# Optimization experiments

Hardware: AMD Instinct MI355X
Metric: run time of the kernel (lower is better)

Reference implementation:

```python
import jax, jax.numpy as jnp
import numpy as np

NUM_BANDS = 8
WINDOW = 2048
OVERLAP = 1024
SR = 16000


def _band_mask(L):
    # Replicates torch: band = searchsorted(band_ranges, |freq|, left) - 1.
    # DC bin gives band=-1 which torch negative-indexes into the LAST band,
    # hence the mod. All bins satisfy band < NUM_BANDS, so all are assigned.
    freqs = np.fft.fftfreq(L, 1.0 / SR)
    ranges = np.linspace(0.0, SR / 2.0, NUM_BANDS + 1)
    idx = np.searchsorted(ranges, np.abs(freqs), side='left') - 1
    idx = idx % NUM_BANDS
    mask = (idx[None, :] == np.arange(NUM_BANDS)[:, None]).astype(np.float32)
    return jnp.asarray(mask)  # [bands, L]


def _band_signals(x):
    # mag*exp(i*phase) of masked bins == masked complex bins; ifft().real per band
    L = x.shape[-1]
    X = jnp.fft.fft(x)                         # [B, L] complex
    mask = _band_mask(L)                       # [bands, L]
    Xb = X[:, None, :] * mask[None, :, :]      # [B, bands, L]
    return jnp.fft.ifft(Xb).real               # [B, bands, L]


def _chunks(sig):
    L = sig.shape[-1]
    hop = WINDOW - OVERLAP
    n = (L - OVERLAP) // hop                   # num_chunks (static)
    idx = (jnp.arange(n) * hop)[:, None] + jnp.arange(WINDOW)[None, :]  # [n, W]
    return sig[:, :, idx]                       # [B, bands, n, W]


def _loudness(x):
    # BS.1770-style energy loudness (vectorized stand-in for the repo's
    # undefined `loudness` helper): -0.691 + 10*log10(mean square)
    ms = jnp.mean(x * x, axis=-1)
    return -0.691 + 10.0 * jnp.log10(ms + 1e-12)


def reference(watermarked_signals, original_signals):
    ro = _band_signals(original_signals)
    rw = _band_signals(watermarked_signals)
    lo = _loudness(_chunks(ro))                # [B, bands, n]
    lw = _loudness(_chunks(rw))
    lo = jnp.where(jnp.isnan(lo), 0.0, lo)
    lw = jnp.where(jnp.isnan(lw), 0.0, lw)
    diff = (lw - lo).reshape(-1)               # ordered (i, j, k) like the torch loop
    w = jax.nn.softmax(diff)
    return jnp.sum(w * diff)


def setup_inputs() -> dict:
    key = jax.random.key(0)
    k1, k2 = jax.random.split(key)
    B, L = 8, 160000
    return {
        'watermarked_signals': jax.random.normal(k1, (B, L), dtype=jnp.float32),
        'original_signals': jax.random.normal(k2, (B, L), dtype=jnp.float32),
    }
```

## Files before the change

kernel.cpp:

```cpp
#include <hip/hip_runtime.h>
#include <hip/hip_fp16.h>
#include <math.h>

constexpr int L      = 160000;
constexpr int BATCH  = 8;
constexpr int NB     = 8;
constexpr int NHOPS  = 156;
constexpr int NCHUNK = 155;
constexpr int RS     = 289;
constexpr float TWO_PI = 6.28318530717958647692f;
constexpr float INVL = 1.0f / (float)L;

__device__ __forceinline__ float2 cmulf(float2 a, float2 b) {
  return make_float2(a.x * b.x - a.y * b.y, a.x * b.y + a.y * b.x);
}

__device__ __forceinline__ float2 cisf(float a) {
  float s, c;
  __sincosf(a, &s, &c);
  return make_float2(c, s);
}

__device__ __forceinline__ int pad8(int i) { return i + (i >> 3); }

template <int SIGN>
__device__ __forceinline__ void bf4s(float2* v) {
  float2 t0 = make_float2(v[0].x + v[2].x, v[0].y + v[2].y);
  float2 t1 = make_float2(v[0].x - v[2].x, v[0].y - v[2].y);
  float2 t2 = make_float2(v[1].x + v[3].x, v[1].y + v[3].y);
  float2 t3 = make_float2(v[1].x - v[3].x, v[1].y - v[3].y);
  v[0] = make_float2(t0.x + t2.x, t0.y + t2.y);
  v[2] = make_float2(t0.x - t2.x, t0.y - t2.y);
  if constexpr (SIGN < 0) {
    v[1] = make_float2(t1.x + t3.y, t1.y - t3.x);
    v[3] = make_float2(t1.x - t3.y, t1.y + t3.x);
  } else {
    v[1] = make_float2(t1.x - t3.y, t1.y + t3.x);
    v[3] = make_float2(t1.x + t3.y, t1.y - t3.x);
  }
}

template <int SIGN>
__device__ __forceinline__ void bf5s(float2* v) {
  const float c1 = 0.30901699437494745f, s1 = 0.9510565162951535f;
  const float c2 = -0.8090169943749475f, s2 = 0.5877852522924731f;
  float2 t1 = make_float2(v[1].x + v[4].x, v[1].y + v[4].y);
  float2 t3 = make_float2(v[1].x - v[4].x, v[1].y - v[4].y);
  float2 t2 = make_float2(v[2].x + v[3].x, v[2].y + v[3].y);
  float2 t4 = make_float2(v[2].x - v[3].x, v[2].y - v[3].y);
  float2 a = make_float2(v[0].x + c1 * t1.x + c2 * t2.x, v[0].y + c1 * t1.y + c2 * t2.y);
  float2 b = make_float2(s1 * t3.x + s2 * t4.x, s1 * t3.y + s2 * t4.y);
  float2 c = make_float2(v[0].x + c2 * t1.x + c1 * t2.x, v[0].y + c2 * t1.y + c1 * t2.y);
  float2 d = make_float2(s2 * t3.x - s1 * t4.x, s2 * t3.y - s1 * t4.y);
  v[0] = make_float2(v[0].x + t1.x + t2.x, v[0].y + t1.y + t2.y);
  if constexpr (SIGN < 0) {
    v[1] = make_float2(a.x + b.y, a.y - b.x);
    v[4] = make_float2(a.x - b.y, a.y + b.x);
    v[2] = make_float2(c.x + d.y, c.y - d.x);
    v[3] = make_float2(c.x - d.y, c.y + d.x);
  } else {
    v[1] = make_float2(a.x - b.y, a.y + b.x);
    v[4] = make_float2(a.x + b.y, a.y - b.x);
    v[2] = make_float2(c.x - d.y, c.y + d.x);
    v[3] = make_float2(c.x + d.y, c.y - d.x);
  }
}

template <int R>
__device__ __forceinline__ void twchain(float2* v, float2 t1) {
  float2 t = t1;
  v[1] = cmulf(v[1], t);
#pragma unroll
  for (int r = 2; r < R; ++r) { t = cmulf(t, t1); v[r] = cmulf(v[r], t); }
}

__device__ __forceinline__ int rev3_5(int q) {
  int q5 = q / 5, q25 = q / 25;
  int d0 = q - 5 * q5, d1 = q5 - 5 * q25;
  return 25 * d0 + 5 * d1 + q25;
}

__device__ __forceinline__ int rev3_4(int q) {
  return ((q & 3) << 4) | (q & 12) | (q >> 4);
}

template <int SUB, int SIGN>
__device__ __forceinline__ void dif5_ip_stage_c(float2* a, int ln) {
  int i1 = ln, i2 = ln + 64;
  bool g2 = (i2 < 125);
  int j1 = i1 % SUB, j2 = i2 % SUB;
  int b1 = (i1 / SUB) * (5 * SUB) + j1;
  int b2 = (i2 / SUB) * (5 * SUB) + j2;
  float2 u[5], v[5];
#pragma unroll
  for (int r = 0; r < 5; ++r) u[r] = a[b1 + SUB * r];
  if (g2) {
#pragma unroll
    for (int r = 0; r < 5; ++r) v[r] = a[b2 + SUB * r];
  }
  bf5s<SIGN>(u);
  twchain<5>(u, cisf((float)SIGN * (TWO_PI / (float)(5 * SUB)) * (float)j1));
  if (g2) {
    bf5s<SIGN>(v);
    twchain<5>(v, cisf((float)SIGN * (TWO_PI / (float)(5 * SUB)) * (float)j2));
  }
#pragma unroll
  for (int r = 0; r < 5; ++r) a[b1 + SUB * r] = u[r];
  if (g2) {
#pragma unroll
    for (int r = 0; r < 5; ++r) a[b2 + SUB * r] = v[r];
  }
}

template <int SUB>
__device__ __forceinline__ void dif5_ip_stage_t(float2* a, int ln, float2 t1a, float2 t1b) {
  int i1 = ln, i2 = ln + 64;
  bool g2 = (i2 < 125);
  int j1 = i1 % SUB, j2 = i2 % SUB;
  int b1 = (i1 / SUB) * (5 * SUB) + j1;
  int b2 = (i2 / SUB) * (5 * SUB) + j2;
  float2 u[5], v[5];
#pragma unroll
  for (int r = 0; r < 5; ++r) u[r] = a[b1 + SUB * r];
  if (g2) {
#pragma unroll
    for (int r = 0; r < 5; ++r) v[r] = a[b2 + SUB * r];
  }
  bf5s<1>(u);
  twchain<5>(u, t1a);
  if (g2) {
    bf5s<1>(v);
    twchain<5>(v, t1b);
  }
#pragma unroll
  for (int r = 0; r < 5; ++r) a[b1 + SUB * r] = u[r];
  if (g2) {
#pragma unroll
    for (int r = 0; r < 5; ++r) a[b2 + SUB * r] = v[r];
  }
}

template <int SIGN>
__device__ __forceinline__ void dif625_ip(float2* a, int ln) {
  dif5_ip_stage_c<125, SIGN>(a, ln);
  dif5_ip_stage_c<25, SIGN>(a, ln);
  dif5_ip_stage_c<5, SIGN>(a, ln);
  int q1 = ln, q2 = ln + 64;
  bool g2 = (q2 < 125);
  float2 u[5], v[5];
#pragma unroll
  for (int r = 0; r < 5; ++r) u[r] = a[5 * q1 + r];
  if (g2) {
#pragma unroll
    for (int r = 0; r < 5; ++r) v[r] = a[5 * q2 + r];
  }
  bf5s<SIGN>(u);
  if (g2) bf5s<SIGN>(v);
  int rv1 = rev3_5(q1), rv2 = rev3_5(q2);
#pragma unroll
  for (int r = 0; r < 5; ++r) a[125 * r + rv1] = u[r];
  if (g2) {
#pragma unroll
    for (int r = 0; r < 5; ++r) a[125 * r + rv2] = v[r];
  }
}

template <int SIGN>
__device__ __forceinline__ void dif256sw_ip(float2* a, int ln) {
  {
    float2 u[4];
#pragma unroll
    for (int r = 0; r < 4; ++r) u[r] = a[pad8(ln + 64 * r)];
    bf4s<SIGN>(u);
    twchain<4>(u, cisf((float)SIGN * (TWO_PI / 256.0f) * (float)ln));
#pragma unroll
    for (int r = 0; r < 4; ++r) a[pad8(ln + 64 * r)] = u[r];
  }
  {
    int j = ln & 15, b = 64 * (ln >> 4) + j;
    float2 u[4];
#pragma unroll
    for (int r = 0; r < 4; ++r) u[r] = a[pad8(b + 16 * r)];
    bf4s<SIGN>(u);
    twchain<4>(u, cisf((float)SIGN * (TWO_PI / 64.0f) * (float)j));
#pragma unroll
    for (int r = 0; r < 4; ++r) a[pad8(b + 16 * r)] = u[r];
  }
  {
    int j = ln & 3, b = 16 * (ln >> 2) + j;
    float2 u[4];
#pragma unroll
    for (int r = 0; r < 4; ++r) u[r] = a[pad8(b + 4 * r)];
    bf4s<SIGN>(u);
    twchain<4>(u, cisf((float)SIGN * (TWO_PI / 16.0f) * (float)j));
#pragma unroll
    for (int r = 0; r < 4; ++r) a[pad8(b + 4 * r)] = u[r];
  }
  {
    float2 u[4];
#pragma unroll
    for (int r = 0; r < 4; ++r) u[r] = a[pad8(4 * ln + r)];
    bf4s<SIGN>(u);
    int rv = rev3_4(ln);
#pragma unroll
    for (int r = 0; r < 4; ++r) a[pad8(64 * r + rv)] = u[r];
  }
}

__global__ __launch_bounds__(256) void f1_kernel(const float* __restrict__ win,
                                                 const float* __restrict__ oin,
                                                 float2* __restrict__ G,
                                                 float* __restrict__ E) {
  __shared__ float2 A[4 * 625];
  int blk = blockIdx.x;
  int gid = blk * 256 + threadIdx.x;
  if (gid < 2 * BATCH * NB * NHOPS) E[gid] = 0.0f;
  int sig = blk >> 6, g = blk & 63;
  int n1base = g * 4;
  int tid = threadIdx.x;
  const float4* wp4 = (const float4*)(win + (size_t)sig * L);
  const float4* op4 = (const float4*)(oin + (size_t)sig * L);
  for (int r = tid; r < 625; r += 256) {
    float4 wv = wp4[r * 64 + g];
    float4 ov = op4[r * 64 + g];
    A[0 * 625 + r] = make_float2(wv.x, ov.x);
    A[1 * 625 + r] = make_float2(wv.y, ov.y);
    A[2 * 625 + r] = make_float2(wv.z, ov.z);
    A[3 * 625 + r] = make_float2(wv.w, ov.w);
  }
  __syncthreads();
  int wv_ = tid >> 6, ln = tid & 63;
  dif625_ip<-1>(A + wv_ * 625, ln);
  __syncthreads();
  int cc = tid & 3, k20 = tid >> 2;
  int n1 = n1base + cc;
  float w = -(TWO_PI / (float)L) * (float)n1;
  float2 t = cisf(w * (float)k20);
  float2 stp = cisf(w * 64.0f);
  for (int k2 = k20; k2 < 625; k2 += 64) {
    G[(size_t)sig * L + k2 * 256 + n1] = cmulf(A[cc * 625 + k2], t);
    t = cmulf(t, stp);
  }
}

__global__ __launch_bounds__(256) void f2_kernel(const float2* __restrict__ G,
                                                 float2* __restrict__ X) {
  __shared__ float2 A[4 * RS];
  int blk = blockIdx.x;
  int sig = blk / 157, gr = blk % 157;
  int k2base = gr * 4;
  int tid = threadIdx.x;
  int wv = tid >> 6, ln = tid & 63;
  int k2 = k2base + wv;
  float2* a = A + wv * RS;
  if (k2 < 625) {
#pragma unroll
    for (int r = 0; r < 4; ++r)
      a[pad8(ln + 64 * r)] = G[(size_t)sig * L + k2 * 256 + ln + 64 * r];
    dif256sw_ip<-1>(a, ln);
  }
  __syncthreads();
  for (int idx = tid; idx < 1024; idx += 256) {
    int row = idx >> 8, k1 = idx & 255;
    int k2e = k2base + row;
    if (k2e < 625) X[(size_t)sig * L + k2e * 256 + k1] = A[row * RS + pad8(k1)];
  }
}

__global__ __launch_bounds__(1024) void i1_kernel(const float2* __restrict__ X,
                                                  __half2* __restrict__ H) {
  __shared__ float2 A[16 * RS];
  int blk = blockIdx.x;
  int gr = blk % 40, sb = blk / 40;
  int band = sb & 7, sig = sb >> 3;
  int k2base = gr * 16;
  int tid = threadIdx.x;
  int wv = tid >> 6, ln = tid & 63;
  int lo1, hi1, lo2, hi2;
  if (band < 7) {
    lo1 = 10000 * band + 1;        hi1 = 10000 * (band + 1);
    lo2 = L - 10000 * (band + 1);  hi2 = L - 10000 * band - 1;
  } else {
    lo1 = 70001; hi1 = 80000; lo2 = 80001; hi2 = 89999;
  }
  float2 zero = make_float2(0.0f, 0.0f);
  int k2 = k2base + wv;
  float2* row = A + wv * RS;
  for (int k1 = ln; k1 < 256; k1 += 64) row[pad8(k1)] = zero;
  if (k2 < 625) {
    const float2* Xr = X + (size_t)sig * L + k2 * 256;
    int s1 = (lo1 - k2 + 624) / 625;
    int e1 = (hi1 - k2) / 625; if (e1 > 255) e1 = 255;
    int s2 = (lo2 - k2 + 624) / 625;
    int e2 = (hi2 - k2) / 625; if (e2 > 255) e2 = 255;
    int c1 = e1 - s1 + 1;
    int c2 = e2 - s2 + 1;
    if (ln < c1) { int k1 = s1 + ln; row[pad8(k1)] = Xr[k1]; }
    int l2 = ln - 32;
    if (l2 >= 0 && l2 < c2) { int k1 = s2 + l2; row[pad8(k1)] = Xr[k1]; }
    if (band == 7 && k2 == 0 && ln == 0) row[pad8(0)] = Xr[0];
    dif256sw_ip<1>(row, ln);
  }
  __syncthreads();
  size_t obase = (size_t)(sig * NB + band) * L;
  int cc = tid & 15, n1g = tid >> 4;
  int k2e = k2base + cc;
  if (k2e < 625) {
    float a0 = (TWO_PI / (float)L) * (float)k2e;
    float2 t = cisf(a0 * (float)n1g);
    float2 stp = cisf(a0 * 64.0f);
#pragma unroll
    for (int it = 0; it < 4; ++it) {
      int n1 = n1g + 64 * it;
      float2 val = cmulf(A[cc * RS + pad8(n1)], t);
      H[obase + (size_t)n1 * 625 + k2e] = __floats2half2_rn(val.x * INVL, val.y * INVL);
      t = cmulf(t, stp);
    }
  }
}

__global__ __launch_bounds__(256) void i2_kernel(const __half2* __restrict__ H,
                                                 float* __restrict__ E) {
  __shared__ float2 A[4 * 625];
  __shared__ float P[4 * 2 * NHOPS];
  int blk = blockIdx.x;
  int g = blk & 31, sb = blk >> 5;
  int band = sb & 7, sig = sb >> 3;
  int tid = threadIdx.x;
  int wv = tid >> 6, ln = tid & 63;
  size_t base = (size_t)(sig * NB + band) * L;
  int n1A = 8 * g + wv, n1B = 8 * g + 4 + wv;
  const __half2* HA = H + base + (size_t)n1A * 625;
  const __half2* HB = H + base + (size_t)n1B * 625;
  int j1 = ln, j2 = ln + 64;
  bool g2 = (j2 < 125);
  __half2 hA1[5], hA2[5], hB1[5], hB2[5];
#pragma unroll
  for (int r = 0; r < 5; ++r) hA1[r] = HA[j1 + 125 * r];
  if (g2) {
#pragma unroll
    for (int r = 0; r < 5; ++r) hA2[r] = HA[j2 + 125 * r];
  }
#pragma unroll
  for (int r = 0; r < 5; ++r) hB1[r] = HB[j1 + 125 * r];
  if (g2) {
#pragma unroll
    for (int r = 0; r < 5; ++r) hB2[r] = HB[j2 + 125 * r];
  }
  float2 tS1a = cisf((TWO_PI / 625.0f) * (float)j1);
  float2 tS1b = cisf((TWO_PI / 625.0f) * (float)j2);
  float2 tS2a = cisf((TWO_PI / 125.0f) * (float)(j1 % 25));
  float2 tS2b = cisf((TWO_PI / 125.0f) * (float)(j2 % 25));
  float2 tS3a = cisf((TWO_PI / 25.0f) * (float)(j1 % 5));
  float2 tS3b = cisf((TWO_PI / 25.0f) * (float)(j2 % 5));
  float2* a = A + wv * 625;
  float* Pw = P + wv * (2 * NHOPS);

  {
    float2 u[5];
#pragma unroll
    for (int r = 0; r < 5; ++r) u[r] = __half22float2(hA1[r]);
    bf5s<1>(u);
    twchain<5>(u, tS1a);
#pragma unroll
    for (int r = 0; r < 5; ++r) a[j1 + 125 * r] = u[r];
    if (g2) {
      float2 v[5];
#pragma unroll
      for (int r = 0; r < 5; ++r) v[r] = __half22float2(hA2[r]);
      bf5s<1>(v);
      twchain<5>(v, tS1b);
#pragma unroll
      for (int r = 0; r < 5; ++r) a[j2 + 125 * r] = v[r];
    }
  }
  dif5_ip_stage_t<25>(a, ln, tS2a, tS2b);
  dif5_ip_stage_t<5>(a, ln, tS3a, tS3b);
  {
    float2 u[5], v[5];
#pragma unroll
    for (int r = 0; r < 5; ++r) u[r] = a[5 * j1 + r];
    if (g2) {
#pragma unroll
      for (int r = 0; r < 5; ++r) v[r] = a[5 * j2 + r];
    }
    bf5s<1>(u);
    if (g2) bf5s<1>(v);
    int rv1 = rev3_5(j1), rv2 = rev3_5(j2);
#pragma unroll
    for (int r = 0; r < 5; ++r) a[125 * r + rv1] = u[r];
    if (g2) {
#pragma unroll
      for (int r = 0; r < 5; ++r) a[125 * r + rv2] = v[r];
    }
  }
  for (int h = ln; h < NHOPS; h += 64) {
    float ex = 0.0f, ey = 0.0f;
#pragma unroll
    for (int d = 0; d < 4; ++d) {
      float2 z = a[4 * h + d];
      ex += z.x * z.x;
      ey += z.y * z.y;
    }
    Pw[h] = ex;
    Pw[NHOPS + h] = ey;
  }

  {
    float2 u[5];
#pragma unroll
    for (int r = 0; r < 5; ++r) u[r] = __half22float2(hB1[r]);
    bf5s<1>(u);
    twchain<5>(u, tS1a);
#pragma unroll
    for (int r = 0; r < 5; ++r) a[j1 + 125 * r] = u[r];
    if (g2) {
      float2 v[5];
#pragma unroll
      for (int r = 0; r < 5; ++r) v[r] = __half22float2(hB2[r]);
      bf5s<1>(v);
      twchain<5>(v, tS1b);
#pragma unroll
      for (int r = 0; r < 5; ++r) a[j2 + 125 * r] = v[r];
    }
  }
  dif5_ip_stage_t<25>(a, ln, tS2a, tS2b);
  dif5_ip_stage_t<5>(a, ln, tS3a, tS3b);
  {
    float2 u[5], v[5];
#pragma unroll
    for (int r = 0; r < 5; ++r) u[r] = a[5 * j1 + r];
    if (g2) {
#pragma unroll
      for (int r = 0; r < 5; ++r) v[r] = a[5 * j2 + r];
    }
    bf5s<1>(u);
    if (g2) bf5s<1>(v);
    int rv1 = rev3_5(j1), rv2 = rev3_5(j2);
#pragma unroll
    for (int r = 0; r < 5; ++r) a[125 * r + rv1] = u[r];
    if (g2) {
#pragma unroll
      for (int r = 0; r < 5; ++r) a[125 * r + rv2] = v[r];
    }
  }
  for (int h = ln; h < NHOPS; h += 64) {
    float ex = 0.0f, ey = 0.0f;
#pragma unroll
    for (int d = 0; d < 4; ++d) {
      float2 z = a[4 * h + d];
      ex += z.x * z.x;
      ey += z.y * z.y;
    }
    Pw[h] += ex;
    Pw[NHOPS + h] += ey;
  }
  __syncthreads();
  int eb = (sig * NB + band) * NHOPS;
  for (int idx = tid; idx < 2 * NHOPS; idx += 256) {
    float v = P[idx] + P[2 * NHOPS + idx] + P[4 * NHOPS + idx] + P[6 * NHOPS + idx];
    int comp = idx / NHOPS, h = idx - comp * NHOPS;
    atomicAdd(&E[comp * (BATCH * NB * NHOPS) + eb + h], v);
  }
}

__global__ __launch_bounds__(1024) void finalize_kernel(const float* __restrict__ E,
                                                        float* __restrict__ out) {
  constexpr int ND = BATCH * NB * NCHUNK;
  constexpr float SC = 1.0f / 2048.0f;
  __shared__ float diffs[ND];
  __shared__ float sred[1024];
  int tid = threadIdx.x;
  for (int idx = tid; idx < ND; idx += 1024) {
    int sb = idx / NCHUNK;
    int k = idx - sb * NCHUNK;
    float msw = (E[sb * NHOPS + k] + E[sb * NHOPS + k + 1]) * SC;
    float mso = (E[64 * NHOPS + sb * NHOPS + k] + E[64 * NHOPS + sb * NHOPS + k + 1]) * SC;
    float lw = -0.691f + 10.0f * log10f(msw + 1e-12f);
    float lo = -0.691f + 10.0f * log10f(mso + 1e-12f);
    diffs[idx] = lw - lo;
  }
  __syncthreads();
  float mx = -3.4e38f;
  for (int idx = tid; idx < ND; idx += 1024) mx = fmaxf(mx, diffs[idx]);
  sred[tid] = mx;
  __syncthreads();
  for (int s = 512; s > 0; s >>= 1) {
    if (tid < s) sred[tid] = fmaxf(sred[tid], sred[tid + s]);
    __syncthreads();
  }
  float gmax = sred[0];
  __syncthreads();
  float se = 0.0f, swd = 0.0f;
  for (int idx = tid; idx < ND; idx += 1024) {
    float d = diffs[idx];
    float e = expf(d - gmax);
    se += e;
    swd += d * e;
  }
  sred[tid] = se; __syncthreads();
  for (int s = 512; s > 0; s >>= 1) { if (tid < s) sred[tid] += sred[tid + s]; __syncthreads(); }
  float tot = sred[0];
  __syncthreads();
  sred[tid] = swd; __syncthreads();
  for (int s = 512; s > 0; s >>= 1) { if (tid < s) sred[tid] += sred[tid + s]; __syncthreads(); }
  if (tid == 0) out[0] = sred[0] / tot;
}

extern "C" void kernel_launch(void* const* d_in, const int* in_sizes, int n_in,
                              void* d_out, int out_size, void* d_ws, size_t ws_size,
                              hipStream_t stream) {
  (void)in_sizes; (void)n_in; (void)out_size; (void)ws_size;
  char* ws = (char*)d_ws;
  float2*  G = (float2*)ws;
  float2*  X = (float2*)(ws + 10240000);
  __half2* H = (__half2*)(ws + 20480000);
  float*   E = (float*)(ws + 61440000);
  const float* w = (const float*)d_in[0];
  const float* o = (const float*)d_in[1];

  f1_kernel<<<dim3(BATCH * 64), dim3(256), 0, stream>>>(w, o, G, E);
  f2_kernel<<<dim3(BATCH * 157), dim3(256), 0, stream>>>(G, X);
  i1_kernel<<<dim3(BATCH * NB * 40), dim3(1024), 0, stream>>>(X, H);
  i2_kernel<<<dim3(BATCH * NB * 32), dim3(256), 0, stream>>>(H, E);
  finalize_kernel<<<dim3(1), dim3(1024), 0, stream>>>(E, (float*)d_out);
}
```

Baseline: 147.5 us.

## Fuse forward second-stage FFT with per-band inverse first stage in shared memory

Merges f2 and i1 into one kernel: each block computes the forward 256-point FFT rows in shared memory, then loops over the 8 bands, masking, inverse-transforming and twiddling in LDS before writing half-precision H. This removes the full float2 X spectrum write and its 8x re-read per band from global memory, along with one kernel launch. In exchange, each block serially processes 8 bands with only 4 rows per block and extra barriers, so parallelism per band drops relative to the old 1024-thread i1 launch.

Measured after the change: 161.4 us. +9.4%, slower.

```diff
diff --git a/kernel.cpp b/kernel.cpp
--- a/kernel.cpp
+++ b/kernel.cpp
@@ -243,79 +243,67 @@
   }
 }
 
-__global__ __launch_bounds__(256) void f2_kernel(const float2* __restrict__ G,
-                                                 float2* __restrict__ X) {
-  __shared__ float2 A[4 * RS];
+__global__ __launch_bounds__(256) void fi_kernel(const float2* __restrict__ G,
+                                                 __half2* __restrict__ H) {
+  __shared__ float2 Xb[4 * RS];
+  __shared__ float2 Wb[4 * RS];
   int blk = blockIdx.x;
   int sig = blk / 157, gr = blk % 157;
   int k2base = gr * 4;
   int tid = threadIdx.x;
   int wv = tid >> 6, ln = tid & 63;
   int k2 = k2base + wv;
-  float2* a = A + wv * RS;
-  if (k2 < 625) {
+  bool act = (k2 < 625);
+  float2* xr = Xb + wv * RS;
+  float2* wr = Wb + wv * RS;
+  if (act) {
 #pragma unroll
     for (int r = 0; r < 4; ++r)
-      a[pad8(ln + 64 * r)] = G[(size_t)sig * L + k2 * 256 + ln + 64 * r];
-    dif256sw_ip<-1>(a, ln);
-  }
-  __syncthreads();
-  for (int idx = tid; idx < 1024; idx += 256) {
-    int row = idx >> 8, k1 = idx & 255;
-    int k2e = k2base + row;
-    if (k2e < 625) X[(size_t)sig * L + k2e * 256 + k1] = A[row * RS + pad8(k1)];
-  }
-}
-
-__global__ __launch_bounds__(1024) void i1_kernel(const float2* __restrict__ X,
-                                                  __half2* __restrict__ H) {
-  __shared__ float2 A[16 * RS];
-  int blk = blockIdx.x;
-  int gr = blk % 40, sb = blk / 40;
-  int band = sb & 7, sig = sb >> 3;
-  int k2base = gr * 16;
-  int tid = threadIdx.x;
-  int wv = tid >> 6, ln = tid & 63;
-  int lo1, hi1, lo2, hi2;
-  if (band < 7) {
-    lo1 = 10000 * band + 1;        hi1 = 10000 * (band + 1);
-    lo2 = L - 10000 * (band + 1);  hi2 = L - 10000 * band - 1;
-  } else {
-    lo1 = 70001; hi1 = 80000; lo2 = 80001; hi2 = 89999;
-  }
+      xr[pad8(ln + 64 * r)] = G[(size_t)sig * L + k2 * 256 + ln + 64 * r];
+    dif256sw_ip<-1>(xr, ln);
+  }
+  int cc = tid & 3, n1g = tid >> 2;
+  int k2e = k2base + cc;
+  float a0 = (TWO_PI / (float)L) * (float)k2e;
+  float2 t0 = cisf(a0 * (float)n1g);
+  float2 stp = cisf(a0 * 64.0f);
   float2 zero = make_float2(0.0f, 0.0f);
-  int k2 = k2base + wv;
-  float2* row = A + wv * RS;
-  for (int k1 = ln; k1 < 256; k1 += 64) row[pad8(k1)] = zero;
-  if (k2 < 625) {
-    const float2* Xr = X + (size_t)sig * L + k2 * 256;
-    int s1 = (lo1 - k2 + 624) / 625;
-    int e1 = (hi1 - k2) / 625; if (e1 > 255) e1 = 255;
-    int s2 = (lo2 - k2 + 624) / 625;
-    int e2 = (hi2 - k2) / 625; if (e2 > 255) e2 = 255;
-    int c1 = e1 - s1 + 1;
-    int c2 = e2 - s2 + 1;
-    if (ln < c1) { int k1 = s1 + ln; row[pad8(k1)] = Xr[k1]; }
-    int l2 = ln - 32;
-    if (l2 >= 0 && l2 < c2) { int k1 = s2 + l2; row[pad8(k1)] = Xr[k1]; }
-    if (band == 7 && k2 == 0 && ln == 0) row[pad8(0)] = Xr[0];
-    dif256sw_ip<1>(row, ln);
-  }
-  __syncthreads();
-  size_t obase = (size_t)(sig * NB + band) * L;
-  int cc = tid & 15, n1g = tid >> 4;
-  int k2e = k2base + cc;
-  if (k2e < 625) {
-    float a0 = (TWO_PI / (float)L) * (float)k2e;
-    float2 t = cisf(a0 * (float)n1g);
-    float2 stp = cisf(a0 * 64.0f);
-#pragma unroll
-    for (int it = 0; it < 4; ++it) {
-      int n1 = n1g + 64 * it;
-      float2 val = cmulf(A[cc * RS + pad8(n1)], t);
-      H[obase + (size_t)n1 * 625 + k2e] = __floats2half2_rn(val.x * INVL, val.y * INVL);
-      t = cmulf(t, stp);
-    }
+
+  for (int band = 0; band < NB; ++band) {
+    int lo1, hi1, lo2, hi2;
+    if (band < 7) {
+      lo1 = 10000 * band + 1;        hi1 = 10000 * (band + 1);
+      lo2 = L - 10000 * (band + 1);  hi2 = L - 10000 * band - 1;
+    } else {
+      lo1 = 70001; hi1 = 80000; lo2 = 80001; hi2 = 89999;
+    }
+    if (act) {
+      for (int k1 = ln; k1 < 256; k1 += 64) wr[pad8(k1)] = zero;
+      int s1 = (lo1 - k2 + 624) / 625;
+      int e1 = (hi1 - k2) / 625; if (e1 > 255) e1 = 255;
+      int s2 = (lo2 - k2 + 624) / 625;
+      int e2 = (hi2 - k2) / 625; if (e2 > 255) e2 = 255;
+      int c1 = e1 - s1 + 1;
+      int c2 = e2 - s2 + 1;
+      if (ln < c1) { int k1 = s1 + ln; wr[pad8(k1)] = xr[pad8(k1)]; }
+      int l2 = ln - 32;
+      if (l2 >= 0 && l2 < c2) { int k1 = s2 + l2; wr[pad8(k1)] = xr[pad8(k1)]; }
+      if (band == 7 && k2 == 0 && ln == 0) wr[pad8(0)] = xr[pad8(0)];
+      dif256sw_ip<1>(wr, ln);
+    }
+    __syncthreads();
+    if (k2e < 625) {
+      size_t obase = (size_t)(sig * NB + band) * L;
+      float2 t = t0;
+#pragma unroll
+      for (int it = 0; it < 4; ++it) {
+        int n1 = n1g + 64 * it;
+        float2 val = cmulf(Wb[cc * RS + pad8(n1)], t);
+        H[obase + (size_t)n1 * 625 + k2e] = __floats2half2_rn(val.x * INVL, val.y * INVL);
+        t = cmulf(t, stp);
+      }
+    }
+    __syncthreads();
   }
 }
 
@@ -513,15 +501,13 @@
   (void)in_sizes; (void)n_in; (void)out_size; (void)ws_size;
   char* ws = (char*)d_ws;
   float2*  G = (float2*)ws;
-  float2*  X = (float2*)(ws + 10240000);
-  __half2* H = (__half2*)(ws + 20480000);
-  float*   E = (float*)(ws + 61440000);
+  __half2* H = (__half2*)(ws + 10240000);
+  float*   E = (float*)(ws + 51200000);
   const float* w = (const float*)d_in[0];
   const float* o = (const float*)d_in[1];
 
   f1_kernel<<<dim3(BATCH * 64), dim3(256), 0, stream>>>(w, o, G, E);
-  f2_kernel<<<dim3(BATCH * 157), dim3(256), 0, stream>>>(G, X);
-  i1_kernel<<<dim3(BATCH * NB * 40), dim3(1024), 0, stream>>>(X, H);
+  fi_kernel<<<dim3(BATCH * 157), dim3(256), 0, stream>>>(G, H);
   i2_kernel<<<dim3(BATCH * NB * 32), dim3(256), 0, stream>>>(H, E);
   finalize_kernel<<<dim3(1), dim3(1024), 0, stream>>>(E, (float*)d_out);
 }
```
